# Kernel optimization log

Hardware: AMD Instinct MI355X
Metric: run time of the kernel (lower is better)

## Reference

```python
import jax, jax.numpy as jnp
import numpy as np

N_NODES = 50000
N_FEAT = 128
DIM = 10
N_EDGES = 1600000
N_GRAPHS = 1000


def setup_inputs() -> dict:
    key = jax.random.key(0)
    ks = jax.random.split(key, 8)
    x = jax.random.normal(ks[0], (N_NODES, N_FEAT), dtype=jnp.float32)
    W1_l = jax.random.normal(ks[1], (DIM, N_FEAT), dtype=jnp.float32) * 0.1
    W1_r = jax.random.normal(ks[2], (DIM, N_FEAT), dtype=jnp.float32) * 0.1
    W2_l = jax.random.normal(ks[3], (DIM, DIM), dtype=jnp.float32) * 0.3
    W2_r = jax.random.normal(ks[4], (DIM, DIM), dtype=jnp.float32) * 0.3
    Wfc = jax.random.normal(ks[5], (1, DIM), dtype=jnp.float32) * 0.3
    edge_index = jax.random.randint(ks[6], (2, N_EDGES), 0, N_NODES, dtype=jnp.int64)
    batch = jnp.sort(jax.random.randint(ks[7], (N_NODES,), 0, N_GRAPHS, dtype=jnp.int64))
    return {"x": x, "W1_l": W1_l, "W1_r": W1_r, "W2_l": W2_l, "W2_r": W2_r,
            "Wfc": Wfc, "edge_index": edge_index, "batch": batch}


def _sage_conv(h, src, dst, deg_inv, Wl, Wr):
    # mean aggregation over incoming neighbors, then two bias-free linears
    agg = jax.ops.segment_sum(h[src], dst, num_segments=N_NODES)  # [N, F]
    agg = agg * deg_inv[:, None]
    return agg @ Wl.T + h @ Wr.T


def reference(x, W1_l, W1_r, W2_l, W2_r, Wfc, edge_index, batch):
    src, dst = edge_index[0], edge_index[1]
    # in-degree per destination node (mean denominator, clamped at 1 like PyG)
    deg = jax.ops.segment_sum(jnp.ones((src.shape[0],), x.dtype), dst, num_segments=N_NODES)
    deg_inv = 1.0 / jnp.maximum(deg, 1.0)

    h = jax.nn.relu(_sage_conv(x, src, dst, deg_inv, W1_l, W1_r))
    h = _sage_conv(h, src, dst, deg_inv, W2_l, W2_r)

    # global mean pool over graphs
    counts = jax.ops.segment_sum(jnp.ones((N_NODES,), x.dtype), batch, num_segments=N_GRAPHS)
    pooled = jax.ops.segment_sum(h, batch, num_segments=N_GRAPHS)
    pooled = pooled / jnp.maximum(counts, 1.0)[:, None]

    return jax.nn.sigmoid(pooled @ Wfc.T)  # [N_GRAPHS, 1]
```

## Files before the change

kernel.cpp:

```cpp
#include <hip/hip_runtime.h>
#include <hip/hip_bf16.h>
#include <math.h>

#define N_NODES  50000
#define N_FEAT   128
#define DIM      10
#define N_EDGES  1600000
#define N_GRAPHS 1000
#define PSTRIDE  16
#define CAP      80
#define BSH      7
#define BNODES   128
#define NBUCK    391
#define BCAP     4608
#define ACHUNK   4096
#define ABLOCKS  ((N_EDGES + ACHUNK - 1) / ACHUNK)
#define PBLOCKS4 ((N_NODES * 4 + 255) / 256)
#define SPLIT    2
#define GSLOTS   128
#define SENT     50000


__device__ __forceinline__ float bf2f(unsigned short u) {
    union { unsigned int i; float f; } v;
    v.i = ((unsigned int)u) << 16;
    return v.f;
}

__device__ __forceinline__ float wload(const void* w, int fm, int i) {
    return fm ? ((const float*)w)[i] : bf2f(((const unsigned short*)w)[i]);
}

__device__ __forceinline__ int iload(const void* p, int im, long long pos) {
    return im ? ((const int*)p)[2 * pos] : ((const int*)p)[pos];
}

__device__ __forceinline__ int probe_fm(const void* W1l) {
    const unsigned short* w = (const unsigned short*)W1l;
    int hits = 0;
#pragma unroll
    for (int i = 0; i < 128; i++) {
        int expo = (w[2 * i] >> 7) & 0xFF;
        hits += (expo >= 0x90) ? 1 : 0;
    }
    return (hits >= 4) ? 1 : 0;
}
__device__ __forceinline__ int probe_im(const void* ei) {
    const unsigned int* e = (const unsigned int*)ei;
    unsigned o = 0;
#pragma unroll
    for (int i = 0; i < 8; i++) o |= e[2 * i + 1];
    return (o == 0) ? 1 : 0;
}

#define ACCUM8(f0)                                                  \
    _Pragma("unroll")                                               \
    for (int d = 0; d < DIM; d++) {                                 \
        _Pragma("unroll")                                           \
        for (int k = 0; k < 8; k++) {                               \
            accl[d] += xf[k] * wl[d * N_FEAT + (f0) + k];           \
            accr[d] += xf[k] * wr[d * N_FEAT + (f0) + k];           \
        }                                                           \
    }

__global__ __launch_bounds__(256) void fusedA_kernel(
    const void* __restrict__ ei, const void* __restrict__ x,
    const void* __restrict__ W1l, const void* __restrict__ W1r,
    int* __restrict__ bcur, unsigned int* __restrict__ bedges,
    float* __restrict__ p, float* __restrict__ q) {
    __shared__ union U {
        struct { int hcnt[NBUCK]; int hbase[NBUCK]; } a;
        struct { float wl[DIM * N_FEAT]; float wr[DIM * N_FEAT]; } b;
    } sh;

    if (blockIdx.x < ABLOCKS) {
        int im = probe_im(ei);
        for (int b = threadIdx.x; b < NBUCK; b += 256) sh.a.hcnt[b] = 0;
        __syncthreads();
        long long e0 = (long long)blockIdx.x * ACHUNK;
        int nE = (int)min((long long)ACHUNK, (long long)N_EDGES - e0);
        for (int i = threadIdx.x; i < nE; i += 256) {
            int d = iload(ei, im, (long long)N_EDGES + e0 + i);
            atomicAdd(&sh.a.hcnt[d >> BSH], 1);
        }
        __syncthreads();
        for (int b = threadIdx.x; b < NBUCK; b += 256) {
            int c = sh.a.hcnt[b];
            sh.a.hbase[b] = c ? atomicAdd(&bcur[b], c) : 0;
            sh.a.hcnt[b] = 0;
        }
        __syncthreads();
        for (int i = threadIdx.x; i < nE; i += 256) {
            int s = iload(ei, im, e0 + i);
            int d = iload(ei, im, (long long)N_EDGES + e0 + i);
            unsigned rec = (unsigned)s | ((unsigned)(d & (BNODES - 1)) << 16) | ((unsigned)(d >> BSH) << 23);
            int b = d >> BSH;
            int pos = sh.a.hbase[b] + atomicAdd(&sh.a.hcnt[b], 1);
            if (pos < BCAP) bedges[(size_t)b * BCAP + pos] = rec;
        }
    } else {
        int fm = probe_fm(W1l);
        if (blockIdx.x == ABLOCKS && threadIdx.x < PSTRIDE)
            p[(size_t)SENT * PSTRIDE + threadIdx.x] = 0.f;
        float* wl = sh.b.wl;
        float* wr = sh.b.wr;
        for (int i = threadIdx.x; i < DIM * N_FEAT; i += 256) {
            wl[i] = wload(W1l, fm, i);
            wr[i] = wload(W1r, fm, i);
        }
        __syncthreads();
        int tid4 = (blockIdx.x - ABLOCKS) * 256 + threadIdx.x;
        int n = tid4 >> 2;
        int sub = tid4 & 3;
        if (n >= N_NODES) return;

        float accl[DIM], accr[DIM];
#pragma unroll
        for (int d = 0; d < DIM; d++) { accl[d] = 0.f; accr[d] = 0.f; }

        if (fm) {
            const float4* xr = reinterpret_cast<const float4*>((const float*)x + (size_t)n * N_FEAT);
#pragma unroll
            for (int j = 0; j < 4; j++) {
                int fb = j * 4 + sub;
                float4 v0 = xr[2 * fb];
                float4 v1 = xr[2 * fb + 1];
                float xf[8] = {v0.x, v0.y, v0.z, v0.w, v1.x, v1.y, v1.z, v1.w};
                ACCUM8(fb * 8)
            }
        } else {
            const uint4* xr = reinterpret_cast<const uint4*>((const unsigned short*)x + (size_t)n * N_FEAT);
#pragma unroll
            for (int j = 0; j < 4; j++) {
                int fb = j * 4 + sub;
                uint4 v = xr[fb];
                float xf[8];
                xf[0] = bf2f((unsigned short)(v.x & 0xffff)); xf[1] = bf2f((unsigned short)(v.x >> 16));
                xf[2] = bf2f((unsigned short)(v.y & 0xffff)); xf[3] = bf2f((unsigned short)(v.y >> 16));
                xf[4] = bf2f((unsigned short)(v.z & 0xffff)); xf[5] = bf2f((unsigned short)(v.z >> 16));
                xf[6] = bf2f((unsigned short)(v.w & 0xffff)); xf[7] = bf2f((unsigned short)(v.w >> 16));
                ACCUM8(fb * 8)
            }
        }
#pragma unroll
        for (int d = 0; d < DIM; d++) {
            accl[d] += __shfl_xor(accl[d], 1, 4);
            accl[d] += __shfl_xor(accl[d], 2, 4);
            accr[d] += __shfl_xor(accr[d], 1, 4);
            accr[d] += __shfl_xor(accr[d], 2, 4);
        }
        if (sub == 0) {
            float4* pr = reinterpret_cast<float4*>(p + (size_t)n * PSTRIDE);
            float4* qr = reinterpret_cast<float4*>(q + (size_t)n * PSTRIDE);
            pr[0] = make_float4(accl[0], accl[1], accl[2], accl[3]);
            pr[1] = make_float4(accl[4], accl[5], accl[6], accl[7]);
            pr[2] = make_float4(accl[8], accl[9], 0.f, 0.f);
            pr[3] = make_float4(0.f, 0.f, 0.f, 0.f);
            qr[0] = make_float4(accr[0], accr[1], accr[2], accr[3]);
            qr[1] = make_float4(accr[4], accr[5], accr[6], accr[7]);
            qr[2] = make_float4(accr[8], accr[9], 0.f, 0.f);
            qr[3] = make_float4(0.f, 0.f, 0.f, 0.f);
        }
    }
}

__global__ __launch_bounds__(512) void pullB_kernel(
    const int* __restrict__ bcur, const unsigned int* __restrict__ bedges,
    const float* __restrict__ p, const float* __restrict__ q,
    const void* __restrict__ W1l, const void* __restrict__ W2l,
    const void* __restrict__ W2r, const void* __restrict__ Wfc,
    float* __restrict__ t, float* __restrict__ u, float* __restrict__ dinv) {
    __shared__ unsigned short lcol[BNODES * CAP];
    __shared__ int lcnt[BNODES];
    __shared__ float svl[16], svr[16];
    int fm = probe_fm(W1l);
    if (threadIdx.x < 16) {
        float al = 0.f, ar = 0.f;
        if (threadIdx.x < DIM) {
            for (int i = 0; i < DIM; i++) {
                float w = wload(Wfc, fm, i);
                al += w * wload(W2l, fm, i * DIM + threadIdx.x);
                ar += w * wload(W2r, fm, i * DIM + threadIdx.x);
            }
        }
        svl[threadIdx.x] = al;
        svr[threadIdx.x] = ar;
    }
    const unsigned int s2 = (unsigned)SENT | ((unsigned)SENT << 16);
    uint4 sv = make_uint4(s2, s2, s2, s2);
    uint4* l4 = reinterpret_cast<uint4*>(lcol);
    for (int i = threadIdx.x; i < BNODES * CAP * 2 / 16; i += 512) l4[i] = sv;
    if (threadIdx.x < BNODES) lcnt[threadIdx.x] = 0;
    __syncthreads();

    int b = blockIdx.x;
    int m = min(bcur[b], BCAP);
    const unsigned int* seg = bedges + (size_t)b * BCAP;
    for (int i = threadIdx.x; i < m; i += 512) {
        unsigned rec = seg[i];
        int nidx = (rec >> 16) & (BNODES - 1);
        int pos = atomicAdd(&lcnt[nidx], 1);
        if (pos < CAP) lcol[nidx * CAP + pos] = (unsigned short)(rec & 0xffffu);
    }
    __syncthreads();

    int n = threadIdx.x >> 2;
    int sub4 = (threadIdx.x & 3) * 4;
    int g = (b << BSH) + n;
    if (g >= N_NODES) return;
    int deg = lcnt[n];
    int dcl = min(deg, CAP);
    const unsigned short* cl = lcol + n * CAP;
    float ax = 0.f, ay = 0.f, az = 0.f, aw = 0.f;
    for (int k0 = 0; k0 < dcl; k0 += 8) {
        uint4 cv = *reinterpret_cast<const uint4*>(cl + k0);
        unsigned c[8];
        c[0] = cv.x & 0xffff; c[1] = cv.x >> 16;
        c[2] = cv.y & 0xffff; c[3] = cv.y >> 16;
        c[4] = cv.z & 0xffff; c[5] = cv.z >> 16;
        c[6] = cv.w & 0xffff; c[7] = cv.w >> 16;
#pragma unroll
        for (int j = 0; j < 8; j++) {
            const float4 v = *reinterpret_cast<const float4*>(p + (size_t)c[j] * PSTRIDE + sub4);
            ax += v.x; ay += v.y; az += v.z; aw += v.w;
        }
    }
    float di = 1.0f / fmaxf((float)deg, 1.0f);
    float4 qv  = *reinterpret_cast<const float4*>(q + (size_t)g * PSTRIDE + sub4);
    float4 vlv = *reinterpret_cast<const float4*>(svl + sub4);
    float4 vrv = *reinterpret_cast<const float4*>(svr + sub4);
    float hx = fmaxf(ax * di + qv.x, 0.f);
    float hy = fmaxf(ay * di + qv.y, 0.f);
    float hz = fmaxf(az * di + qv.z, 0.f);
    float hw = fmaxf(aw * di + qv.w, 0.f);
    float tv = hx * vlv.x + hy * vlv.y + hz * vlv.z + hw * vlv.w;
    float uv = hx * vrv.x + hy * vrv.y + hz * vrv.z + hw * vrv.w;
    tv += __shfl_xor(tv, 1, 4); tv += __shfl_xor(tv, 2, 4);
    uv += __shfl_xor(uv, 1, 4); uv += __shfl_xor(uv, 2, 4);
    if ((threadIdx.x & 3) == 0) {
        t[g] = tv;
        u[g] = uv;
        dinv[g] = di;
    }
}

__global__ __launch_bounds__(256) void pull2B_kernel(
    const int* __restrict__ bcur, const unsigned int* __restrict__ bedges,
    const float* __restrict__ t, const float* __restrict__ u,
    const float* __restrict__ dinv, const void* __restrict__ batch,
    const void* __restrict__ ei,
    float* __restrict__ gsum, float* __restrict__ gcnt) {
    __shared__ float lnode[BNODES];
    __shared__ float ldinv[BNODES];
    __shared__ int   lb[BNODES];
    __shared__ float lgs[GSLOTS];
    __shared__ float lgc[GSLOTS];
    int im = probe_im(ei);
    int b = blockIdx.x / SPLIT;
    int s = blockIdx.x % SPLIT;
    int tid = threadIdx.x;
    int node0 = b << BSH;
    int nvalid = min(BNODES, N_NODES - node0);
    if (tid < BNODES) lnode[tid] = 0.f;
    if (tid < nvalid) {
        ldinv[tid] = dinv[node0 + tid];
        lb[tid] = iload(batch, im, node0 + tid);
    }
    if (tid < GSLOTS) { lgs[tid] = 0.f; lgc[tid] = 0.f; }
    __syncthreads();
    int m = min(bcur[b], BCAP);
    int c0 = (m * s) / SPLIT, c1 = (m * (s + 1)) / SPLIT;
    const unsigned int* seg = bedges + (size_t)b * BCAP;
    for (int i = c0 + tid; i < c1; i += 256) {
        unsigned rec = seg[i];
        int src  = rec & 0xffffu;
        int nidx = (rec >> 16) & (BNODES - 1);
        atomicAdd(&lnode[nidx], t[src]);
    }
    __syncthreads();
    int g0 = lb[0];
    int rng = lb[nvalid - 1] - g0 + 1;
    bool useLDS = (rng <= GSLOTS);
    if (tid < nvalid) {
        float gv = lnode[tid] * ldinv[tid];
        if (s == 0) gv += u[node0 + tid];
        int gg = lb[tid];
        if (useLDS) {
            atomicAdd(&lgs[gg - g0], gv);
            if (s == 0) atomicAdd(&lgc[gg - g0], 1.0f);
        } else {
            if (gv != 0.f) atomicAdd(gsum + gg, gv);
            if (s == 0) atomicAdd(gcnt + gg, 1.0f);
        }
    }
    __syncthreads();
    if (useLDS) {
        for (int i = tid; i < rng; i += 256) {
            float v = lgs[i];
            if (v != 0.f) atomicAdd(gsum + g0 + i, v);
            if (s == 0) {
                float c = lgc[i];
                if (c != 0.f) atomicAdd(gcnt + g0 + i, c);
            }
        }
    }
}

__global__ __launch_bounds__(256) void final_kernel(
    const float* __restrict__ gsum, const float* __restrict__ gcnt,
    const void* __restrict__ W1l, void* __restrict__ out) {
    int fm = probe_fm(W1l);
    int g = blockIdx.x * 256 + threadIdx.x;
    if (g >= N_GRAPHS) return;
    float pooled = gsum[g] / fmaxf(gcnt[g], 1.0f);
    float sg = 1.0f / (1.0f + expf(-pooled));
    if (fm) {
        ((float*)out)[g] = sg;
    } else {
        ((__hip_bfloat16*)out)[g] = __float2bfloat16(sg);
    }
}

extern "C" void kernel_launch(void* const* d_in, const int* in_sizes, int n_in,
                              void* d_out, int out_size, void* d_ws, size_t ws_size,
                              hipStream_t stream) {
    const void* x    = d_in[0];
    const void* W1l  = d_in[1];
    const void* W1r  = d_in[2];
    const void* W2l  = d_in[3];
    const void* W2r  = d_in[4];
    const void* Wfc  = d_in[5];
    const void* ei   = d_in[6];
    const void* batc = d_in[7];

    char* ws = (char*)d_ws;
    int*   bcur = (int*)ws;
    float* gsum = (float*)(bcur + NBUCK);
    float* gcnt = gsum + N_GRAPHS;
    unsigned int* bedges = (unsigned int*)(ws + ((((size_t)(gcnt + N_GRAPHS) - (size_t)ws) + 255) & ~(size_t)255));
    float* p    = (float*)(bedges + (size_t)NBUCK * BCAP);
    float* q    = p + (size_t)(N_NODES + 1) * PSTRIDE;
    float* t    = q + (size_t)N_NODES * PSTRIDE;
    float* u    = t + N_NODES;
    float* dinv = u + N_NODES;

    hipMemsetAsync(bcur, 0, (NBUCK + 2 * N_GRAPHS) * sizeof(int), stream);
    fusedA_kernel<<<ABLOCKS + PBLOCKS4, 256, 0, stream>>>(
        ei, x, W1l, W1r, bcur, bedges, p, q);
    pullB_kernel<<<NBUCK, 512, 0, stream>>>(bcur, bedges, p, q,
                                            W1l, W2l, W2r, Wfc, t, u, dinv);
    pull2B_kernel<<<NBUCK * SPLIT, 256, 0, stream>>>(bcur, bedges, t, u, dinv, batc, ei, gsum, gcnt);
    final_kernel<<<(N_GRAPHS + 255) / 256, 256, 0, stream>>>(gsum, gcnt, W1l, d_out);
}
```

Measured before the change: 163.9 us.

## Stage edge binning through LDS counting sort for coalesced bucket writes

The edge-binning pass now reads each edge once into shared memory, counts per bucket, computes an exclusive scan, and scatters records into a bucket-sorted LDS buffer. Global bucket stores then go out as contiguous runs instead of as scattered atomics-driven writes. Chunk size is halved and the second pull kernel's split is doubled for more parallelism. The per-thread dtype probes are replaced by wave-wide ballot probes to cut redundant loads. The cost is more LDS use and more block-wide barriers.

New measurement: 174.4 us. 6.4% more time.

```diff
diff --git a/kernel.cpp b/kernel.cpp
--- a/kernel.cpp
+++ b/kernel.cpp
@@ -13,10 +13,10 @@
 #define BNODES   128
 #define NBUCK    391
 #define BCAP     4608
-#define ACHUNK   4096
+#define ACHUNK   2048
 #define ABLOCKS  ((N_EDGES + ACHUNK - 1) / ACHUNK)
 #define PBLOCKS4 ((N_NODES * 4 + 255) / 256)
-#define SPLIT    2
+#define SPLIT    4
 #define GSLOTS   128
 #define SENT     50000
 
@@ -35,22 +35,19 @@
     return im ? ((const int*)p)[2 * pos] : ((const int*)p)[pos];
 }
 
-__device__ __forceinline__ int probe_fm(const void* W1l) {
+__device__ __forceinline__ int probe_fm_w(const void* W1l) {
     const unsigned short* w = (const unsigned short*)W1l;
-    int hits = 0;
-#pragma unroll
-    for (int i = 0; i < 128; i++) {
-        int expo = (w[2 * i] >> 7) & 0xFF;
-        hits += (expo >= 0x90) ? 1 : 0;
-    }
-    return (hits >= 4) ? 1 : 0;
-}
-__device__ __forceinline__ int probe_im(const void* ei) {
+    int lane = threadIdx.x & 63;
+    int expo = (w[lane] >> 7) & 0xFF;
+    unsigned long long m = __ballot(expo >= 0x90);
+    return (__popcll(m) >= 4) ? 1 : 0;
+}
+__device__ __forceinline__ int probe_im_w(const void* ei) {
     const unsigned int* e = (const unsigned int*)ei;
-    unsigned o = 0;
-#pragma unroll
-    for (int i = 0; i < 8; i++) o |= e[2 * i + 1];
-    return (o == 0) ? 1 : 0;
+    int lane = threadIdx.x & 63;
+    unsigned v = (lane < 8) ? e[2 * lane + 1] : 0u;
+    unsigned long long m = __ballot(v != 0u);
+    return (m == 0ull) ? 1 : 0;
 }
 
 #define ACCUM8(f0)                                                  \
@@ -69,37 +66,62 @@
     int* __restrict__ bcur, unsigned int* __restrict__ bedges,
     float* __restrict__ p, float* __restrict__ q) {
     __shared__ union U {
-        struct { int hcnt[NBUCK]; int hbase[NBUCK]; } a;
+        struct { unsigned int stage[ACHUNK]; unsigned int stage2[ACHUNK];
+                 int cur[NBUCK]; int adj[NBUCK]; } a;
         struct { float wl[DIM * N_FEAT]; float wr[DIM * N_FEAT]; } b;
     } sh;
+    __shared__ int wsum[4];
 
     if (blockIdx.x < ABLOCKS) {
-        int im = probe_im(ei);
-        for (int b = threadIdx.x; b < NBUCK; b += 256) sh.a.hcnt[b] = 0;
+        int im = probe_im_w(ei);
+        for (int b = threadIdx.x; b < NBUCK; b += 256) sh.a.cur[b] = 0;
         __syncthreads();
         long long e0 = (long long)blockIdx.x * ACHUNK;
         int nE = (int)min((long long)ACHUNK, (long long)N_EDGES - e0);
         for (int i = threadIdx.x; i < nE; i += 256) {
-            int d = iload(ei, im, (long long)N_EDGES + e0 + i);
-            atomicAdd(&sh.a.hcnt[d >> BSH], 1);
-        }
-        __syncthreads();
-        for (int b = threadIdx.x; b < NBUCK; b += 256) {
-            int c = sh.a.hcnt[b];
-            sh.a.hbase[b] = c ? atomicAdd(&bcur[b], c) : 0;
-            sh.a.hcnt[b] = 0;
-        }
-        __syncthreads();
-        for (int i = threadIdx.x; i < nE; i += 256) {
             int s = iload(ei, im, e0 + i);
             int d = iload(ei, im, (long long)N_EDGES + e0 + i);
-            unsigned rec = (unsigned)s | ((unsigned)(d & (BNODES - 1)) << 16) | ((unsigned)(d >> BSH) << 23);
-            int b = d >> BSH;
-            int pos = sh.a.hbase[b] + atomicAdd(&sh.a.hcnt[b], 1);
-            if (pos < BCAP) bedges[(size_t)b * BCAP + pos] = rec;
+            sh.a.stage[i] = (unsigned)s | ((unsigned)(d & (BNODES - 1)) << 16) | ((unsigned)(d >> BSH) << 23);
+            atomicAdd(&sh.a.cur[d >> BSH], 1);
+        }
+        __syncthreads();
+        int t = threadIdx.x;
+        int b0 = 2 * t, b1 = 2 * t + 1;
+        int c0 = (b0 < NBUCK) ? sh.a.cur[b0] : 0;
+        int c1 = (b1 < NBUCK) ? sh.a.cur[b1] : 0;
+        int hb0 = c0 ? atomicAdd(&bcur[b0], c0) : 0;
+        int hb1 = c1 ? atomicAdd(&bcur[b1], c1) : 0;
+        int s = c0 + c1;
+        int inc = s;
+        int lane = t & 63;
+#pragma unroll
+        for (int off = 1; off < 64; off <<= 1) {
+            int v = __shfl_up(inc, off);
+            if (lane >= off) inc += v;
+        }
+        if (lane == 63) wsum[t >> 6] = inc;
+        __syncthreads();
+        int wbase = 0;
+        for (int w = 0; w < (t >> 6); w++) wbase += wsum[w];
+        int excl = wbase + inc - s;
+        __syncthreads();
+        if (b0 < NBUCK) { sh.a.cur[b0] = excl;      sh.a.adj[b0] = hb0 - excl; }
+        if (b1 < NBUCK) { sh.a.cur[b1] = excl + c0; sh.a.adj[b1] = hb1 - (excl + c0); }
+        __syncthreads();
+        for (int i = threadIdx.x; i < nE; i += 256) {
+            unsigned rec = sh.a.stage[i];
+            int pos = atomicAdd(&sh.a.cur[rec >> 23], 1);
+            sh.a.stage2[pos] = rec;
+        }
+        __syncthreads();
+        for (int k = threadIdx.x; k < nE; k += 256) {
+            unsigned rec = sh.a.stage2[k];
+            int b = rec >> 23;
+            int gi = sh.a.adj[b] + k;
+            if (gi < BCAP) bedges[(size_t)b * BCAP + gi] = rec;
         }
     } else {
-        int fm = probe_fm(W1l);
+        int fm = probe_fm_w(W1l);
         if (blockIdx.x == ABLOCKS && threadIdx.x < PSTRIDE)
             p[(size_t)SENT * PSTRIDE + threadIdx.x] = 0.f;
         float* wl = sh.b.wl;
@@ -173,7 +195,7 @@
     __shared__ unsigned short lcol[BNODES * CAP];
     __shared__ int lcnt[BNODES];
     __shared__ float svl[16], svr[16];
-    int fm = probe_fm(W1l);
+    int fm = probe_fm_w(W1l);
     if (threadIdx.x < 16) {
         float al = 0.f, ar = 0.f;
         if (threadIdx.x < DIM) {
@@ -255,7 +277,7 @@
     __shared__ int   lb[BNODES];
     __shared__ float lgs[GSLOTS];
     __shared__ float lgc[GSLOTS];
-    int im = probe_im(ei);
+    int im = probe_im_w(ei);
     int b = blockIdx.x / SPLIT;
     int s = blockIdx.x % SPLIT;
     int tid = threadIdx.x;
@@ -309,7 +331,7 @@
 __global__ __launch_bounds__(256) void final_kernel(
     const float* __restrict__ gsum, const float* __restrict__ gcnt,
     const void* __restrict__ W1l, void* __restrict__ out) {
-    int fm = probe_fm(W1l);
+    int fm = probe_fm_w(W1l);
     int g = blockIdx.x * 256 + threadIdx.x;
     if (g >= N_GRAPHS) return;
     float pooled = gsum[g] / fmaxf(gcnt[g], 1.0f);
```
